# Performance work log

Hardware: AMD Instinct MI355X
Metric: run time of the kernel (lower is better)

The kernel has to match this reference:

```python
import jax, jax.numpy as jnp
import numpy as np
import math

N, I, C, T, V, M = 256, 2, 6, 300, 25, 2
D = 256
IN_DIM = I * C * T * V * M  # 180000


def _const_mats():
    a = math.radians(30.0)
    ca, sa = math.cos(a), math.sin(a)
    R_x = np.array([[1, 0, 0], [0, ca, sa], [0, -sa, ca]], np.float32).T
    R_y = np.array([[ca, 0, -sa], [0, 1, 0], [sa, 0, ca]], np.float32).T
    R_z = np.array([[ca, sa, 0], [-sa, ca, 0], [0, 0, 1]], np.float32).T
    R_rotate = R_x @ R_y @ R_z
    R_scale = np.diag([2.0, 2.0, 2.0]).astype(np.float32)
    R_shear = np.ones((3, 3), np.float32)  # sh_next=1 -> all ones (transpose is identity op)
    return R_rotate, R_shear, R_scale


def _param_mats():
    rotate_w = np.zeros((3, 3), np.float32)
    rotate_w[0, 0] = 1.0
    rotate_w[1, 1] = rotate_w[1, 2] = rotate_w[2, 1] = rotate_w[2, 2] = 0.7
    shear_w = np.full((3, 3), 0.8, np.float32)
    np.fill_diagonal(shear_w, 1.0)
    scale_w = np.diag([0.6, 0.6, 0.6]).astype(np.float32)
    return rotate_w, shear_w, scale_w


def setup_inputs() -> dict:
    key = jax.random.key(0)
    k1, k2 = jax.random.split(key)
    R_rotate, R_shear, R_scale = _const_mats()
    rotate_w, shear_w, scale_w = _param_mats()
    x = jax.random.normal(k1, (N, I, C, T, V, M), jnp.float32)
    W = jax.random.normal(k2, (IN_DIM, D), jnp.float32) * (1.0 / math.sqrt(IN_DIM))
    b = jnp.zeros((D,), jnp.float32)
    return {
        "x": x,
        "rotate_weight": jnp.asarray(rotate_w),
        "shear_weight": jnp.asarray(shear_w),
        "scale_weight": jnp.asarray(scale_w),
        "W_backbone": W,
        "b_backbone": b,
        "R_rotate": jnp.asarray(R_rotate),
        "R_shear": jnp.asarray(R_shear),
        "R_scale": jnp.asarray(R_scale),
    }


def _loss_fn(q, z, n):
    q = q / jnp.linalg.norm(q, axis=-1, keepdims=True)
    z = z / jnp.linalg.norm(z, axis=-1, keepdims=True)
    sim = q @ z.T                       # [N, N]
    diag = jnp.diagonal(sim)            # (q*z).sum(-1)
    offdiag_sum = sim.sum(axis=-1) - diag
    return diag - offdiag_sum / (n - 1)


def reference(x, rotate_weight, shear_weight, scale_weight, W_backbone, b_backbone,
              R_rotate, R_shear, R_scale):
    n, i, c, t, v, m = x.shape
    # per-pass effective 3x3 matrices (elementwise gated constants)
    Rr = R_rotate * rotate_weight
    Rs = R_shear * shear_weight
    Rc = R_scale * scale_weight
    Rtot = Rr @ Rs @ Rc  # sequential passes compose: y @ Rr @ Rs @ Rc
    # split C=6 into two xyz chunks, rotate coord axis (vectorized over N,I,chunk,T,V,M)
    xr = x.reshape(n, i, 2, 3, t, v, m)
    x_aug = jnp.einsum("nhctvm,cd->nhdtvm", xr.reshape(n * i, 2 * 0 + 2, 3, t, v, m)[0:0] if False else xr.reshape(n, i * 2, 3, t, v, m), Rtot)
    x_aug = x_aug.reshape(n, i, c, t, v, m)
    # torch x1 = x aliases: x2 == x1 == augmented tensor -> both branches identical
    feats = x_aug.reshape(n, -1)
    z = feats @ W_backbone + b_backbone  # backbone; projector(num_layers=0) is identity
    out = z                              # out1 == out2 == z
    q = z                                # predictor is identity
    z_d = jax.lax.stop_gradient(z)
    loss = _loss_fn(q, z_d, n) + _loss_fn(q, z_d, n)
    return (loss.mean(), out, out)
```

## Files before the change

### kernel.cpp

```cpp
#include <hip/hip_runtime.h>

typedef __attribute__((ext_vector_type(4))) short bf16x4;
typedef __attribute__((ext_vector_type(8))) short bf16x8;
typedef __attribute__((ext_vector_type(16))) float f32x16;
typedef __attribute__((ext_vector_type(2))) float f32x2;
typedef __attribute__((ext_vector_type(4))) unsigned int u32x4;

__device__ __forceinline__ unsigned short f2bf(float f) {
    unsigned int u = __builtin_bit_cast(unsigned int, f);
    u += 0x7fffu + ((u >> 16) & 1u);
    return (unsigned short)(u >> 16);
}

#define PA 196

__global__ __launch_bounds__(512, 2) void gemm_kernel(
    const float* __restrict__ x,
    const float* __restrict__ rw, const float* __restrict__ sw, const float* __restrict__ cw,
    const float* __restrict__ W,
    const float* __restrict__ Rr, const float* __restrict__ Rs, const float* __restrict__ Rc,
    float* __restrict__ P)
{
    __shared__ unsigned short lds_a[256 * PA];
    __shared__ unsigned int   lds_b[2][16 * 256];

    const int tid = threadIdx.x;
    const int blk = blockIdx.x;
    const int p0 = blk * 60;

    float Ar[9], Br[9], Cr[9], T1[9], RT[9];
    #pragma unroll
    for (int e = 0; e < 9; ++e) {
        Ar[e] = Rr[e] * rw[e];
        Br[e] = Rs[e] * sw[e];
        Cr[e] = Rc[e] * cw[e];
    }
    #pragma unroll
    for (int r = 0; r < 3; ++r)
        #pragma unroll
        for (int c = 0; c < 3; ++c)
            T1[r*3+c] = Ar[r*3+0]*Br[0*3+c] + Ar[r*3+1]*Br[1*3+c] + Ar[r*3+2]*Br[2*3+c];
    #pragma unroll
    for (int r = 0; r < 3; ++r)
        #pragma unroll
        for (int c = 0; c < 3; ++c)
            RT[r*3+c] = T1[r*3+0]*Cr[0*3+c] + T1[r*3+1]*Cr[1*3+c] + T1[r*3+2]*Cr[2*3+c];

    if (tid < 256) {
        bf16x4 zz = (bf16x4)0;
        #pragma unroll
        for (int c3 = 0; c3 < 3; ++c3)
            *((bf16x4*)&lds_a[tid*PA + c3*64 + 60]) = zz;
    }

    const int w  = tid >> 6, l = tid & 63;
    const int lm = l & 31,  lh = l >> 5;
    const int m0 = (w >> 1) * 64;
    const int d0 = (w & 1) * 128;

    f32x16 acc[2][4];
    #pragma unroll
    for (int fm = 0; fm < 2; ++fm)
        #pragma unroll
        for (int fd = 0; fd < 4; ++fd)
            acc[fm][fd] = (f32x16)0.0f;

    for (int s = 0; s < 4; ++s) {
        const int i = s >> 1, chunk = s & 1;
        const long kbase = (long)i * 90000 + (long)chunk * 45000 + p0;
        const float* xs = x + kbase;

        f32x2 L0[4], L1[4];
        int bd[4], bvk2[4];
        #pragma unroll
        for (int jj = 0; jj < 4; ++jj) {
            int item = jj*512 + tid;
            int vk2l = item >> 7, dp = item & 127;
            int vk = vk2l*2;
            int c3 = vk >> 6, pl = vk & 63;
            bd[jj] = dp*2; bvk2[jj] = vk2l;
            L0[jj] = (f32x2){0.f,0.f}; L1[jj] = (f32x2){0.f,0.f};
            if (pl < 60) {
                const float* wr = W + (kbase + (long)c3*15000 + pl)*256 + dp*2;
                L0[jj] = *(const f32x2*)wr;
                L1[jj] = *(const f32x2*)(wr + 256);
            }
        }

        #pragma unroll 6
        for (int j = 0; j < 30; ++j) {
            int q = j*512 + tid;
            int n = (int)(((unsigned)q * 34953u) >> 21);
            int pl = q - n*60;
            const float* px = xs + (long)n*180000 + pl;
            float x0 = px[0], x1 = px[15000], x2 = px[30000];
            float f0 = x0*RT[0] + x1*RT[3] + x2*RT[6];
            float f1 = x0*RT[1] + x1*RT[4] + x2*RT[7];
            float f2 = x0*RT[2] + x1*RT[5] + x2*RT[8];
            int a = n*PA + pl;
            lds_a[a      ] = f2bf(f0);
            lds_a[a +  64] = f2bf(f1);
            lds_a[a + 128] = f2bf(f2);
        }

        #pragma unroll
        for (int jj = 0; jj < 4; ++jj) {
            unsigned int lo = (unsigned int)f2bf(L0[jj].x) | ((unsigned int)f2bf(L1[jj].x) << 16);
            unsigned int hi = (unsigned int)f2bf(L0[jj].y) | ((unsigned int)f2bf(L1[jj].y) << 16);
            unsigned int* pb = &lds_b[0][bvk2[jj]*256 + bd[jj]];
            pb[0] = lo; pb[1] = hi;
        }
        __syncthreads();

        for (int t = 0; t < 6; ++t) {
            f32x2 M0[4], M1[4];
            int cd[4], cvk2[4];
            const bool have = (t < 5);
            if (have) {
                #pragma unroll
                for (int jj = 0; jj < 4; ++jj) {
                    int item = jj*512 + tid;
                    int vk2l = item >> 7, dp = item & 127;
                    int vk = (t+1)*32 + vk2l*2;
                    int c3 = vk >> 6, pl = vk & 63;
                    cd[jj] = dp*2; cvk2[jj] = vk2l;
                    M0[jj] = (f32x2){0.f,0.f}; M1[jj] = (f32x2){0.f,0.f};
                    if (pl < 60) {
                        const float* wr = W + (kbase + (long)c3*15000 + pl)*256 + dp*2;
                        M0[jj] = *(const f32x2*)wr;
                        M1[jj] = *(const f32x2*)(wr + 256);
                    }
                }
            }

            const unsigned int* bbuf = lds_b[t & 1];
            #pragma unroll
            for (int kk = 0; kk < 2; ++kk) {
                int vk0 = t*32 + kk*16;
                int kb = vk0 + lh*8;
                bf16x8 af[2];
                #pragma unroll
                for (int fm = 0; fm < 2; ++fm) {
                    const unsigned short* pa = &lds_a[(m0 + fm*32 + lm)*PA + kb];
                    bf16x4 alo = *(const bf16x4*)pa;
                    bf16x4 ahi = *(const bf16x4*)(pa + 4);
                    af[fm] = __builtin_shufflevector(alo, ahi, 0,1,2,3,4,5,6,7);
                }
                #pragma unroll
                for (int fd = 0; fd < 4; ++fd) {
                    int db = d0 + fd*32 + lm;
                    int v2 = kk*8 + lh*4;
                    u32x4 bw = { bbuf[(v2+0)*256 + db], bbuf[(v2+1)*256 + db],
                                 bbuf[(v2+2)*256 + db], bbuf[(v2+3)*256 + db] };
                    bf16x8 bfv = __builtin_bit_cast(bf16x8, bw);
                    #pragma unroll
                    for (int fm = 0; fm < 2; ++fm)
                        acc[fm][fd] = __builtin_amdgcn_mfma_f32_32x32x16_bf16(af[fm], bfv, acc[fm][fd], 0, 0, 0);
                }
            }

            if (have) {
                unsigned int* nb = &lds_b[(t+1) & 1][0];
                #pragma unroll
                for (int jj = 0; jj < 4; ++jj) {
                    unsigned int lo = (unsigned int)f2bf(M0[jj].x) | ((unsigned int)f2bf(M1[jj].x) << 16);
                    unsigned int hi = (unsigned int)f2bf(M0[jj].y) | ((unsigned int)f2bf(M1[jj].y) << 16);
                    unsigned int* pb = &nb[cvk2[jj]*256 + cd[jj]];
                    pb[0] = lo; pb[1] = hi;
                }
            }
            __syncthreads();
        }
    }

    float* Pb = P + (size_t)blk * 65536;
    #pragma unroll
    for (int fm = 0; fm < 2; ++fm)
        #pragma unroll
        for (int fd = 0; fd < 4; ++fd)
            #pragma unroll
            for (int r = 0; r < 16; ++r) {
                int row = m0 + fm*32 + (r & 3) + 8*(r >> 2) + 4*lh;
                int col = d0 + fd*32 + lm;
                Pb[row*256 + col] = acc[fm][fd][r];
            }
}

__global__ __launch_bounds__(1024) void reduce_kernel(
    const float* __restrict__ P, const float* __restrict__ bias,
    float* __restrict__ out, float* __restrict__ Z)
{
    __shared__ float sred[4][256];
    __shared__ float wsum[16];
    const int n = blockIdx.x;
    const int tid = threadIdx.x;
    const int sg = tid >> 8, d = tid & 255;

    const float* p = P + (size_t)n*256 + d;
    float z = 0.f;
    #pragma unroll 8
    for (int s = sg; s < 250; s += 4) z += p[(size_t)s * 65536];
    sred[sg][d] = z;
    __syncthreads();

    float zf = 0.f;
    if (sg == 0) zf = sred[0][d] + sred[1][d] + sred[2][d] + sred[3][d] + bias[d];
    float sq = zf * zf;
    #pragma unroll
    for (int off = 32; off > 0; off >>= 1) sq += __shfl_down(sq, off, 64);
    if ((tid & 63) == 0) wsum[tid >> 6] = sq;
    __syncthreads();
    if (sg == 0) {
        float tot = wsum[0] + wsum[1] + wsum[2] + wsum[3];
        float inv = rsqrtf(tot);
        out[1 + n*256 + d]         = zf;
        out[1 + 65536 + n*256 + d] = zf;
        Z[n*256 + d] = zf * inv;
    }
}

__global__ __launch_bounds__(1024) void loss_kernel(const float* __restrict__ Z, float* __restrict__ out)
{
    __shared__ float sp[4][256];
    __shared__ float w4[16];
    const int tid = threadIdx.x;
    const int g = tid >> 8, d = tid & 255;
    float S = 0.f;
    #pragma unroll 8
    for (int n = g*64; n < g*64 + 64; ++n) S += Z[n*256 + d];
    sp[g][d] = S;
    __syncthreads();
    float v = 0.f;
    if (g == 0) {
        S = sp[0][d] + sp[1][d] + sp[2][d] + sp[3][d];
        v = S * S;
    }
    #pragma unroll
    for (int off = 32; off > 0; off >>= 1) v += __shfl_down(v, off, 64);
    if ((tid & 63) == 0) w4[tid >> 6] = v;
    __syncthreads();
    if (tid == 0) {
        float tot = w4[0] + w4[1] + w4[2] + w4[3];
        out[0] = 2.0f - (2.0f / 255.0f) * (tot * (1.0f / 256.0f) - 1.0f);
    }
}

extern "C" void kernel_launch(void* const* d_in, const int* in_sizes, int n_in,
                              void* d_out, int out_size, void* d_ws, size_t ws_size,
                              hipStream_t stream)
{
    (void)in_sizes; (void)n_in; (void)out_size; (void)ws_size;
    const float* x  = (const float*)d_in[0];
    const float* rw = (const float*)d_in[1];
    const float* sw = (const float*)d_in[2];
    const float* cw = (const float*)d_in[3];
    const float* W  = (const float*)d_in[4];
    const float* bb = (const float*)d_in[5];
    const float* Rr = (const float*)d_in[6];
    const float* Rs = (const float*)d_in[7];
    const float* Rc = (const float*)d_in[8];
    float* out = (float*)d_out;
    float* P = (float*)d_ws;
    float* Z = P + (size_t)250 * 65536;

    gemm_kernel<<<250, 512, 0, stream>>>(x, rw, sw, cw, W, Rr, Rs, Rc, P);
    reduce_kernel<<<256, 1024, 0, stream>>>(P, bb, out, Z);
    loss_kernel<<<1, 1024, 0, stream>>>(Z, out);
}
```

Measured before the change: 408.2 us.

## Deepen W prefetch pipeline across slabs and vectorize x/W global loads

```diff
diff --git a/kernel.cpp b/kernel.cpp
--- a/kernel.cpp
+++ b/kernel.cpp
@@ -3,7 +3,7 @@
 typedef __attribute__((ext_vector_type(4))) short bf16x4;
 typedef __attribute__((ext_vector_type(8))) short bf16x8;
 typedef __attribute__((ext_vector_type(16))) float f32x16;
-typedef __attribute__((ext_vector_type(2))) float f32x2;
+typedef __attribute__((ext_vector_type(4))) float f32x4;
 typedef __attribute__((ext_vector_type(4))) unsigned int u32x4;
 
 __device__ __forceinline__ unsigned short f2bf(float f) {
@@ -13,6 +13,90 @@
 }
 
 #define PA 196
+
+#define ISSUE(RW, kb, sub) do { \
+    _Pragma("unroll") \
+    for (int jj_ = 0; jj_ < 2; ++jj_) { \
+        const int vk2_ = jj_*8 + (tid >> 6); \
+        const int vk_  = (sub)*32 + vk2_*2; \
+        const int c3_  = vk_ >> 6, pl_ = vk_ & 63; \
+        f32x4 q0_ = {0.f,0.f,0.f,0.f}, q1_ = {0.f,0.f,0.f,0.f}; \
+        if (pl_ < 60) { \
+            const float* wr_ = W + ((kb) + (long)c3_*15000 + pl_)*256 + (tid & 63)*4; \
+            q0_ = *(const f32x4*)wr_; \
+            q1_ = *(const f32x4*)(wr_ + 256); \
+        } \
+        RW[jj_*8+0]=q0_.x; RW[jj_*8+1]=q0_.y; RW[jj_*8+2]=q0_.z; RW[jj_*8+3]=q0_.w; \
+        RW[jj_*8+4]=q1_.x; RW[jj_*8+5]=q1_.y; RW[jj_*8+6]=q1_.z; RW[jj_*8+7]=q1_.w; \
+    } \
+} while (0)
+
+#define PACK(RW, bufsel) do { \
+    _Pragma("unroll") \
+    for (int jj_ = 0; jj_ < 2; ++jj_) { \
+        const int vk2_ = jj_*8 + (tid >> 6); \
+        u32x4 pw_; \
+        pw_.x = (unsigned)f2bf(RW[jj_*8+0]) | ((unsigned)f2bf(RW[jj_*8+4]) << 16); \
+        pw_.y = (unsigned)f2bf(RW[jj_*8+1]) | ((unsigned)f2bf(RW[jj_*8+5]) << 16); \
+        pw_.z = (unsigned)f2bf(RW[jj_*8+2]) | ((unsigned)f2bf(RW[jj_*8+6]) << 16); \
+        pw_.w = (unsigned)f2bf(RW[jj_*8+3]) | ((unsigned)f2bf(RW[jj_*8+7]) << 16); \
+        *((u32x4*)&lds_b[bufsel][vk2_*256 + (tid & 63)*4]) = pw_; \
+    } \
+} while (0)
+
+#define ASTAGE(kb) do { \
+    const float* xs_ = x + (kb); \
+    _Pragma("unroll 2") \
+    for (int k_ = 0; k_ < 8; ++k_) { \
+        const int it_ = k_*512 + tid; \
+        if (it_ < 3840) { \
+            const int n_  = (int)(((unsigned)it_ * 4370u) >> 16);   \
+            const int pl_ = (it_ - n_*15) * 4; \
+            const float* px_ = xs_ + (long)n_*180000 + pl_; \
+            const f32x4 c0_ = *(const f32x4*)px_; \
+            const f32x4 c1_ = *(const f32x4*)(px_ + 15000); \
+            const f32x4 c2_ = *(const f32x4*)(px_ + 30000); \
+            bf16x4 o0_, o1_, o2_; \
+            _Pragma("unroll") \
+            for (int e_ = 0; e_ < 4; ++e_) { \
+                o0_[e_] = (short)f2bf(c0_[e_]*RT[0] + c1_[e_]*RT[3] + c2_[e_]*RT[6]); \
+                o1_[e_] = (short)f2bf(c0_[e_]*RT[1] + c1_[e_]*RT[4] + c2_[e_]*RT[7]); \
+                o2_[e_] = (short)f2bf(c0_[e_]*RT[2] + c1_[e_]*RT[5] + c2_[e_]*RT[8]); \
+            } \
+            const int a_ = n_*PA + pl_; \
+            *(bf16x4*)&lds_a[a_      ] = o0_; \
+            *(bf16x4*)&lds_a[a_ +  64] = o1_; \
+            *(bf16x4*)&lds_a[a_ + 128] = o2_; \
+        } \
+    } \
+} while (0)
+
+#define MFMASTEP(jstep) do { \
+    const unsigned int* bb_ = lds_b[(jstep) & 1]; \
+    _Pragma("unroll") \
+    for (int kk_ = 0; kk_ < 2; ++kk_) { \
+        const int kb_ = (jstep)*32 + kk_*16 + lh*8; \
+        bf16x8 af_[2]; \
+        _Pragma("unroll") \
+        for (int fm_ = 0; fm_ < 2; ++fm_) { \
+            const unsigned short* pa_ = &lds_a[(m0 + fm_*32 + lm)*PA + kb_]; \
+            bf16x4 alo_ = *(const bf16x4*)pa_; \
+            bf16x4 ahi_ = *(const bf16x4*)(pa_ + 4); \
+            af_[fm_] = __builtin_shufflevector(alo_, ahi_, 0,1,2,3,4,5,6,7); \
+        } \
+        _Pragma("unroll") \
+        for (int fd_ = 0; fd_ < 4; ++fd_) { \
+            const int db_ = d0 + fd_*32 + lm; \
+            const int v2_ = kk_*8 + lh*4; \
+            u32x4 bw_ = { bb_[(v2_+0)*256 + db_], bb_[(v2_+1)*256 + db_], \
+                          bb_[(v2_+2)*256 + db_], bb_[(v2_+3)*256 + db_] }; \
+            bf16x8 bv_ = __builtin_bit_cast(bf16x8, bw_); \
+            _Pragma("unroll") \
+            for (int fm_ = 0; fm_ < 2; ++fm_) \
+                acc[fm_][fd_] = __builtin_amdgcn_mfma_f32_32x32x16_bf16(af_[fm_], bv_, acc[fm_][fd_], 0, 0, 0); \
+        } \
+    } \
+} while (0)
 
 __global__ __launch_bounds__(512, 2) void gemm_kernel(
     const float* __restrict__ x,
@@ -65,109 +149,36 @@
         for (int fd = 0; fd < 4; ++fd)
             acc[fm][fd] = (f32x16)0.0f;
 
-    for (int s = 0; s < 4; ++s) {
-        const int i = s >> 1, chunk = s & 1;
-        const long kbase = (long)i * 90000 + (long)chunk * 45000 + p0;
-        const float* xs = x + kbase;
-
-        f32x2 L0[4], L1[4];
-        int bd[4], bvk2[4];
-        #pragma unroll
-        for (int jj = 0; jj < 4; ++jj) {
-            int item = jj*512 + tid;
-            int vk2l = item >> 7, dp = item & 127;
-            int vk = vk2l*2;
-            int c3 = vk >> 6, pl = vk & 63;
-            bd[jj] = dp*2; bvk2[jj] = vk2l;
-            L0[jj] = (f32x2){0.f,0.f}; L1[jj] = (f32x2){0.f,0.f};
-            if (pl < 60) {
-                const float* wr = W + (kbase + (long)c3*15000 + pl)*256 + dp*2;
-                L0[jj] = *(const f32x2*)wr;
-                L1[jj] = *(const f32x2*)(wr + 256);
-            }
-        }
-
-        #pragma unroll 6
-        for (int j = 0; j < 30; ++j) {
-            int q = j*512 + tid;
-            int n = (int)(((unsigned)q * 34953u) >> 21);
-            int pl = q - n*60;
-            const float* px = xs + (long)n*180000 + pl;
-            float x0 = px[0], x1 = px[15000], x2 = px[30000];
-            float f0 = x0*RT[0] + x1*RT[3] + x2*RT[6];
-            float f1 = x0*RT[1] + x1*RT[4] + x2*RT[7];
-            float f2 = x0*RT[2] + x1*RT[5] + x2*RT[8];
-            int a = n*PA + pl;
-            lds_a[a      ] = f2bf(f0);
-            lds_a[a +  64] = f2bf(f1);
-            lds_a[a + 128] = f2bf(f2);
-        }
-
-        #pragma unroll
-        for (int jj = 0; jj < 4; ++jj) {
-            unsigned int lo = (unsigned int)f2bf(L0[jj].x) | ((unsigned int)f2bf(L1[jj].x) << 16);
-            unsigned int hi = (unsigned int)f2bf(L0[jj].y) | ((unsigned int)f2bf(L1[jj].y) << 16);
-            unsigned int* pb = &lds_b[0][bvk2[jj]*256 + bd[jj]];
-            pb[0] = lo; pb[1] = hi;
-        }
-        __syncthreads();
-
-        for (int t = 0; t < 6; ++t) {
-            f32x2 M0[4], M1[4];
-            int cd[4], cvk2[4];
-            const bool have = (t < 5);
-            if (have) {
-                #pragma unroll
-                for (int jj = 0; jj < 4; ++jj) {
-                    int item = jj*512 + tid;
-                    int vk2l = item >> 7, dp = item & 127;
-                    int vk = (t+1)*32 + vk2l*2;
-                    int c3 = vk >> 6, pl = vk & 63;
-                    cd[jj] = dp*2; cvk2[jj] = vk2l;
-                    M0[jj] = (f32x2){0.f,0.f}; M1[jj] = (f32x2){0.f,0.f};
-                    if (pl < 60) {
-                        const float* wr = W + (kbase + (long)c3*15000 + pl)*256 + dp*2;
-                        M0[jj] = *(const f32x2*)wr;
-                        M1[jj] = *(const f32x2*)(wr + 256);
-                    }
-                }
-            }
-
-            const unsigned int* bbuf = lds_b[t & 1];
-            #pragma unroll
-            for (int kk = 0; kk < 2; ++kk) {
-                int vk0 = t*32 + kk*16;
-                int kb = vk0 + lh*8;
-                bf16x8 af[2];
-                #pragma unroll
-                for (int fm = 0; fm < 2; ++fm) {
-                    const unsigned short* pa = &lds_a[(m0 + fm*32 + lm)*PA + kb];
-                    bf16x4 alo = *(const bf16x4*)pa;
-                    bf16x4 ahi = *(const bf16x4*)(pa + 4);
-                    af[fm] = __builtin_shufflevector(alo, ahi, 0,1,2,3,4,5,6,7);
-                }
-                #pragma unroll
-                for (int fd = 0; fd < 4; ++fd) {
-                    int db = d0 + fd*32 + lm;
-                    int v2 = kk*8 + lh*4;
-                    u32x4 bw = { bbuf[(v2+0)*256 + db], bbuf[(v2+1)*256 + db],
-                                 bbuf[(v2+2)*256 + db], bbuf[(v2+3)*256 + db] };
-                    bf16x8 bfv = __builtin_bit_cast(bf16x8, bw);
-                    #pragma unroll
-                    for (int fm = 0; fm < 2; ++fm)
-                        acc[fm][fd] = __builtin_amdgcn_mfma_f32_32x32x16_bf16(af[fm], bfv, acc[fm][fd], 0, 0, 0);
-                }
-            }
-
-            if (have) {
-                unsigned int* nb = &lds_b[(t+1) & 1][0];
-                #pragma unroll
-                for (int jj = 0; jj < 4; ++jj) {
-                    unsigned int lo = (unsigned int)f2bf(M0[jj].x) | ((unsigned int)f2bf(M1[jj].x) << 16);
-                    unsigned int hi = (unsigned int)f2bf(M0[jj].y) | ((unsigned int)f2bf(M1[jj].y) << 16);
-                    unsigned int* pb = &nb[cvk2[jj]*256 + cd[jj]];
-                    pb[0] = lo; pb[1] = hi;
-                }
+    float RWa[16], RWb[16];
+
+    ISSUE(RWa, (long)p0, 0);
+    ASTAGE((long)p0);
+    ISSUE(RWb, (long)p0, 1);
+    PACK(RWa, 0);
+    __syncthreads();
+
+    for (int slab = 0; slab < 4; ++slab) {
+        const long kbase = (long)slab * 45000 + p0;
+        const long kbnxt = kbase + 45000;
+        #pragma unroll
+        for (int j = 0; j < 6; ++j) {
+            if (j < 4) {
+                if (j & 1) ISSUE(RWb, kbase, j+2);
+                else       ISSUE(RWa, kbase, j+2);
+            } else if (slab < 3) {
+                if (j & 1) ISSUE(RWb, kbnxt, j-4);
+                else       ISSUE(RWa, kbnxt, j-4);
+            }
+            if (j == 0 && slab > 0) {
+                ASTAGE(kbase);
+                __syncthreads();
+            }
+            MFMASTEP(j);
+            if (j < 5) {
+                if (j & 1) PACK(RWa, ((j+1)&1));
+                else       PACK(RWb, ((j+1)&1));
+            } else if (slab < 3) {
+                PACK(RWa, 0);
             }
             __syncthreads();
         }
```

Measured after the change: 412.1 us. About the same (+1.0%).
